# Performance work log

Hardware: AMD Instinct MI355X
Metric: run time of the kernel (lower is better)

## Reference

```python
import jax, jax.numpy as jnp
import numpy as np
from jax import lax

B, N, D, H, K = 8, 1024, 384, 6, 7
HD = D // H
EPS = 1e-5


def layer_norm(x, g, b):
    m = jnp.mean(x, axis=-1, keepdims=True)
    v = jnp.mean(jnp.square(x - m), axis=-1, keepdims=True)
    return (x - m) * lax.rsqrt(v + EPS) * g + b


def setup_inputs() -> dict:
    key = jax.random.key(0)
    ks = jax.random.split(key, 12)
    s = 0.02
    return {
        "x": jax.random.normal(ks[0], (B, N, D), jnp.float32),
        "qkv_w": jax.random.normal(ks[1], (3 * D, D), jnp.float32) * s,
        "qkv_b": jnp.zeros((3 * D,), jnp.float32),
        "proj_w": jax.random.normal(ks[2], (D, D), jnp.float32) * s,
        "proj_b": jnp.zeros((D,), jnp.float32),
        "t_before": jnp.eye(H, dtype=jnp.float32) + jax.random.normal(ks[3], (H, H), jnp.float32) * 0.01,
        "t_after": jnp.eye(H, dtype=jnp.float32) + jax.random.normal(ks[4], (H, H), jnp.float32) * 0.01,
        "dw_w": jax.random.normal(ks[5], (D, 1, K), jnp.float32) * s,
        "dw_b": jnp.zeros((D,), jnp.float32),
        "mlp_ln_g": jnp.ones((D,), jnp.float32),
        "mlp_ln_b": jnp.zeros((D,), jnp.float32),
        "norm1_g": jnp.ones((D,), jnp.float32),
        "norm1_b": jnp.zeros((D,), jnp.float32),
        "norm2_g": jnp.ones((D,), jnp.float32),
        "norm2_b": jnp.zeros((D,), jnp.float32),
        "fc1_w": jax.random.normal(ks[6], (4 * D, D), jnp.float32) * s,
        "fc1_b": jnp.zeros((4 * D,), jnp.float32),
        "fc2_w": jax.random.normal(ks[7], (D, 4 * D), jnp.float32) * s,
        "fc2_b": jnp.zeros((D,), jnp.float32),
    }


def reference(x, qkv_w, qkv_b, proj_w, proj_b, t_before, t_after, dw_w, dw_b,
              mlp_ln_g, mlp_ln_b, norm1_g, norm1_b, norm2_g, norm2_b,
              fc1_w, fc1_b, fc2_w, fc2_b):
    # ---- attention branch ----
    h = layer_norm(x, norm1_g, norm1_b)
    qkv = h @ qkv_w.T + qkv_b                                  # (B,N,3D)
    qkv = qkv.reshape(B, N, 3, H, HD).transpose(2, 0, 3, 1, 4)  # (3,B,H,N,hd)
    q, k, v = qkv[0], qkv[1], qkv[2]
    scale = HD ** -0.5
    scores = jnp.einsum('bhnd,bhmd->bhnm', q, k) * scale        # (B,H,N,N)
    scores = jnp.einsum('gh,bhnm->bgnm', t_before, scores)       # head-mix pre-softmax
    probs = jax.nn.softmax(scores, axis=-1)
    probs = jnp.einsum('gh,bhnm->bgnm', t_after, probs)          # head-mix post-softmax
    attn_out = jnp.einsum('bhnm,bhmd->bhnd', probs, v)           # (B,H,N,hd)
    attn_out = attn_out.transpose(0, 2, 1, 3).reshape(B, N, D)
    attn_out = attn_out @ proj_w.T + proj_b
    x = x + attn_out
    # ---- MLP branch ----
    h = layer_norm(x, norm2_g, norm2_b)
    # depthwise conv1d over tokens: (B,D,N), groups=D, same padding
    h_t = h.transpose(0, 2, 1)
    h_t = lax.conv_general_dilated(h_t, dw_w, window_strides=(1,),
                                   padding=[(K // 2, K // 2)],
                                   dimension_numbers=('NCH', 'OIH', 'NCH'),
                                   feature_group_count=D)
    h = h_t.transpose(0, 2, 1) + dw_b
    h = layer_norm(h, mlp_ln_g, mlp_ln_b)
    h = jax.nn.gelu(h @ fc1_w.T + fc1_b, approximate=False)
    h = h @ fc2_w.T + fc2_b
    return x + h
```

## Files before the change

kernel.cpp:

```cpp
#include <hip/hip_runtime.h>
#include <hip/hip_bf16.h>

#define BB 8
#define NN 1024
#define DD 384
#define HH 6
#define HD 64
#define BN 8192
#define D3 1152
#define D4 1536
#define SEC 3145728

typedef __attribute__((ext_vector_type(8))) short short8;
typedef __attribute__((ext_vector_type(4))) float f32x4;
typedef __attribute__((ext_vector_type(2))) float f32x2;
typedef long v2i64 __attribute__((ext_vector_type(2)));

typedef __attribute__((address_space(3))) unsigned char as3_byte;
typedef __attribute__((address_space(1))) const unsigned char as1_byte;

__device__ __forceinline__ void gload16(const void* g, void* l){
  __builtin_amdgcn_global_load_lds((as1_byte*)g, (as3_byte*)l, 16, 0, 0);
}

__device__ __forceinline__ float b2f(unsigned short u){
  union{unsigned int i; float f;} x; x.i=((unsigned int)u)<<16; return x.f;
}
__device__ __forceinline__ unsigned short f2b(float f){
  unsigned int u=__float_as_uint(f);
  return (unsigned short)((u + 0x7FFFu + ((u>>16)&1u))>>16);
}
__device__ __forceinline__ unsigned char f2f8(float f){
  return (unsigned char)(__builtin_amdgcn_cvt_pk_fp8_f32(f, f, 0, false) & 0xff);
}

__global__ void cvt_kernel(const float* __restrict__ w0, const float* __restrict__ w1,
                           const float* __restrict__ w2, const float* __restrict__ w3,
                           unsigned char* __restrict__ out8){
  int i = blockIdx.x*256 + threadIdx.x;
  if (i < 442368)        out8[i] = f2f8(w0[i]*8.0f);
  else if (i < 589824)   out8[i] = f2f8(w1[i - 442368]*8.0f);
  else if (i < 1179648)  out8[i] = f2f8(w2[i - 589824]*8.0f);
  else if (i < 1769472)  out8[i] = f2f8(w3[i - 1179648]*8.0f);
}

template<int OUT8>
__global__ __launch_bounds__(128)
void ln_kernel(const float* __restrict__ in, const float* __restrict__ gg, const float* __restrict__ bb,
               unsigned short* __restrict__ outb, unsigned char* __restrict__ out8){
  int row = blockIdx.x, t = threadIdx.x;
  const float* r = in + (size_t)row*DD;
  float v0=r[t], v1=r[t+128], v2=r[t+256];
  float s=v0+v1+v2, q=v0*v0+v1*v1+v2*v2;
  #pragma unroll
  for (int o=32;o>0;o>>=1){ s+=__shfl_down(s,o); q+=__shfl_down(q,o); }
  __shared__ float ls[2], lq[2];
  if ((t&63)==0){ ls[t>>6]=s; lq[t>>6]=q; }
  __syncthreads();
  float S=ls[0]+ls[1], Q=lq[0]+lq[1];
  float mean=S*(1.0f/DD);
  float rstd=rsqrtf(Q*(1.0f/DD)-mean*mean+1e-5f);
  float o0=(v0-mean)*rstd*gg[t]+bb[t];
  float o1=(v1-mean)*rstd*gg[t+128]+bb[t+128];
  float o2=(v2-mean)*rstd*gg[t+256]+bb[t+256];
  if (OUT8){
    unsigned char* o=out8+(size_t)row*DD;
    o[t]=f2f8(o0*4.0f); o[t+128]=f2f8(o1*4.0f); o[t+256]=f2f8(o2*4.0f);
  } else {
    unsigned short* o=outb+(size_t)row*DD;
    o[t]=f2b(o0); o[t+128]=f2b(o1); o[t+256]=f2b(o2);
  }
}

__global__ __launch_bounds__(128)
void conv_ln_kernel(const unsigned short* __restrict__ h2, const float* __restrict__ dww, const float* __restrict__ dwb,
                    const float* __restrict__ gg, const float* __restrict__ bb, unsigned char* __restrict__ out8){
  int row=blockIdx.x, t=threadIdx.x;
  int bi=row>>10, n=row&1023;
  const unsigned short* base = h2 + (size_t)(bi<<10)*DD;
  float a[3];
  #pragma unroll
  for (int j=0;j<3;j++){
    int d=t+j*128;
    float acc=dwb[d];
    #pragma unroll
    for (int k=0;k<7;k++){
      int nn=n+k-3;
      if (nn>=0 && nn<NN) acc += dww[d*7+k]*b2f(base[(size_t)nn*DD + d]);
    }
    a[j]=acc;
  }
  float s=a[0]+a[1]+a[2], q=a[0]*a[0]+a[1]*a[1]+a[2]*a[2];
  #pragma unroll
  for (int o=32;o>0;o>>=1){ s+=__shfl_down(s,o); q+=__shfl_down(q,o); }
  __shared__ float ls[2], lq[2];
  if ((t&63)==0){ ls[t>>6]=s; lq[t>>6]=q; }
  __syncthreads();
  float S=ls[0]+ls[1], Q=lq[0]+lq[1];
  float mean=S*(1.0f/DD);
  float rstd=rsqrtf(Q*(1.0f/DD)-mean*mean+1e-5f);
  unsigned char* o = out8 + (size_t)row*DD;
  #pragma unroll
  for (int j=0;j<3;j++){
    int d=t+j*128;
    o[d]=f2f8(((a[j]-mean)*rstd*gg[d]+bb[d])*4.0f);
  }
}

template<int MODE>
__global__ __launch_bounds__(256)
void gemm8_kernel(const unsigned char* __restrict__ A8, const unsigned char* __restrict__ W8,
                  const float* __restrict__ bias, const float* __restrict__ resid,
                  float* __restrict__ outf, unsigned char* __restrict__ out8,
                  unsigned char* __restrict__ qk8out, unsigned char* __restrict__ v8out,
                  int Kdim, int Ncols){
  __shared__ __align__(16) unsigned char As[2][64*64];
  __shared__ __align__(16) unsigned char Bs[2][64*64];
  int t=threadIdx.x, lane=t&63, w=t>>6;
  int bm = blockIdx.x*64;
  int bn = blockIdx.y*64;
  int wr = w>>1, wc = w&1;
  int c16=lane&15, r16=lane>>4;
  f32x4 acc[2][2] = {};
  int arow = t>>2, aslot = (t&3) ^ (arow&3);
  auto stage = [&](int buf, int k0){
    gload16(A8 + (size_t)(bm+arow)*Kdim + k0 + aslot*16, (char*)As + buf*4096 + t*16);
    gload16(W8 + (size_t)(bn+arow)*Kdim + k0 + aslot*16, (char*)Bs + buf*4096 + t*16);
  };
  int niter = Kdim>>6;
  stage(0, 0);
  __syncthreads();
  for (int it=0; it<niter; ++it){
    if (it+1<niter) stage((it+1)&1, (it+1)<<6);
    int off = (it&1)*4096;
    #pragma unroll
    for (int kk=0;kk<2;kk++){
      long afr[2], bfr[2];
      #pragma unroll
      for (int i=0;i<2;i++){
        int ra = wr*32 + i*16 + c16;
        int sa = (kk*2 + (r16>>1)) ^ (ra&3);
        afr[i] = *(const long*)((char*)As + off + ra*64 + (sa<<4) + ((r16&1)<<3));
        int rb = wc*32 + i*16 + c16;
        int sb = (kk*2 + (r16>>1)) ^ (rb&3);
        bfr[i] = *(const long*)((char*)Bs + off + rb*64 + (sb<<4) + ((r16&1)<<3));
      }
      #pragma unroll
      for (int i=0;i<2;i++)
        #pragma unroll
        for (int j=0;j<2;j++)
          acc[i][j] = __builtin_amdgcn_mfma_f32_16x16x32_fp8_fp8(afr[i], bfr[j], acc[i][j], 0,0,0);
    }
    __syncthreads();
  }
  #pragma unroll
  for (int i=0;i<2;i++)
    #pragma unroll
    for (int j=0;j<2;j++)
      #pragma unroll
      for (int r=0;r<4;r++){
        int row = bm + wr*32 + i*16 + r16*4 + r;
        int col = bn + wc*32 + j*16 + c16;
        float v = acc[i][j][r]*0.03125f + bias[col];
        if (MODE==0){
          int c = col/384; int rem = col - c*384; int hh = rem>>6, d = rem&63;
          int bi = row>>10, nn = row&1023;
          unsigned char pk = f2f8(v);
          if (c==2){
            v8out[(((size_t)(bi*6+hh))<<16) + ((size_t)d<<10) + nn] = pk;
          } else {
            size_t fa = ((size_t)c*SEC)
                      + ((((size_t)(bi*6+hh))<<6) + (nn>>4))*1024
                      + ((((d>>3)&3)*16 + (nn&15))<<4) + ((d>>5)*8) + (d&7);
            qk8out[fa] = pk;
          }
        } else if (MODE==1){
          size_t idx = (size_t)row*Ncols + col;
          outf[idx] = resid[idx] + v;
        } else {
          float ge = 0.5f*v*(1.0f+erff(v*0.70710678118654752f));
          out8[(size_t)row*Ncols + col] = f2f8(ge*4.0f);
        }
      }
}

__global__ __launch_bounds__(256, 4)
void smx_kernel(const unsigned char* __restrict__ qk8, const float* __restrict__ tbm,
                unsigned char* __restrict__ E, float* __restrict__ lpart){
  __shared__ float lred[4][6][16];
  int t=threadIdx.x, lane=t&63, w=t>>6;
  int blk=blockIdx.x;
  int b = blk&7, nt = (blk>>3)&63, mh = blk>>9;
  int n0 = nt*16, mbase = mh*512;
  int c16=lane&15, r16=lane>>4;
  const unsigned char* q8f = qk8;
  const unsigned char* k8f = qk8 + SEC;
  v2i64 qf[6];
  #pragma unroll
  for (int h=0;h<6;h++)
    qf[h] = *(const v2i64*)(q8f + (((((size_t)(b*6+h))<<6) + (n0>>4))<<10) + lane*16);
  float tbr[36];
  #pragma unroll
  for (int i=0;i<36;i++) tbr[i] = tbm[i];
  const float SC = 0.125f*1.44269504088896f;
  float lsum[6]={0.f,0.f,0.f,0.f,0.f,0.f};
  #pragma unroll
  for (int mt=0; mt<4; ++mt){
    int m0a = mbase + mt*128 + w*16;
    int m0b = m0a + 64;
    v2i64 kfa[6], kfb[6];
    #pragma unroll
    for (int h=0;h<6;h++)
      kfa[h] = *(const v2i64*)(k8f + (((((size_t)(b*6+h))<<6) + (m0a>>4))<<10) + lane*16);
    #pragma unroll
    for (int h=0;h<6;h++)
      kfb[h] = *(const v2i64*)(k8f + (((((size_t)(b*6+h))<<6) + (m0b>>4))<<10) + lane*16);
    {
      f32x4 aq[6] = {};
      #pragma unroll
      for (int h=0;h<6;h++){
        aq[h] = __builtin_amdgcn_mfma_f32_16x16x32_fp8_fp8(kfa[h][0], qf[h][0], aq[h], 0,0,0);
        aq[h] = __builtin_amdgcn_mfma_f32_16x16x32_fp8_fp8(kfa[h][1], qf[h][1], aq[h], 0,0,0);
      }
      #pragma unroll
      for (int g=0;g<6;g++){
        float e0,e1,e2,e3;
        {
          float sm;
          sm = tbr[g*6]*aq[0][0]+tbr[g*6+1]*aq[1][0]+tbr[g*6+2]*aq[2][0]
             + tbr[g*6+3]*aq[3][0]+tbr[g*6+4]*aq[4][0]+tbr[g*6+5]*aq[5][0];
          e0 = __builtin_amdgcn_exp2f(sm*SC);
          sm = tbr[g*6]*aq[0][1]+tbr[g*6+1]*aq[1][1]+tbr[g*6+2]*aq[2][1]
             + tbr[g*6+3]*aq[3][1]+tbr[g*6+4]*aq[4][1]+tbr[g*6+5]*aq[5][1];
          e1 = __builtin_amdgcn_exp2f(sm*SC);
          sm = tbr[g*6]*aq[0][2]+tbr[g*6+1]*aq[1][2]+tbr[g*6+2]*aq[2][2]
             + tbr[g*6+3]*aq[3][2]+tbr[g*6+4]*aq[4][2]+tbr[g*6+5]*aq[5][2];
          e2 = __builtin_amdgcn_exp2f(sm*SC);
          sm = tbr[g*6]*aq[0][3]+tbr[g*6+1]*aq[1][3]+tbr[g*6+2]*aq[2][3]
             + tbr[g*6+3]*aq[3][3]+tbr[g*6+4]*aq[4][3]+tbr[g*6+5]*aq[5][3];
          e3 = __builtin_amdgcn_exp2f(sm*SC);
        }
        lsum[g] += (e0+e1)+(e2+e3);
        int pkv = __builtin_amdgcn_cvt_pk_fp8_f32(e0, e1, 0, false);
        pkv = __builtin_amdgcn_cvt_pk_fp8_f32(e2, e3, pkv, true);
        *(unsigned int*)(E + (((size_t)(b*6+g))<<20) + ((size_t)(n0+c16)<<10) + m0a + r16*4)
          = (unsigned int)pkv;
      }
    }
    {
      f32x4 aq[6] = {};
      #pragma unroll
      for (int h=0;h<6;h++){
        aq[h] = __builtin_amdgcn_mfma_f32_16x16x32_fp8_fp8(kfb[h][0], qf[h][0], aq[h], 0,0,0);
        aq[h] = __builtin_amdgcn_mfma_f32_16x16x32_fp8_fp8(kfb[h][1], qf[h][1], aq[h], 0,0,0);
      }
      #pragma unroll
      for (int g=0;g<6;g++){
        float e0,e1,e2,e3;
        {
          float sm;
          sm = tbr[g*6]*aq[0][0]+tbr[g*6+1]*aq[1][0]+tbr[g*6+2]*aq[2][0]
             + tbr[g*6+3]*aq[3][0]+tbr[g*6+4]*aq[4][0]+tbr[g*6+5]*aq[5][0];
          e0 = __builtin_amdgcn_exp2f(sm*SC);
          sm = tbr[g*6]*aq[0][1]+tbr[g*6+1]*aq[1][1]+tbr[g*6+2]*aq[2][1]
             + tbr[g*6+3]*aq[3][1]+tbr[g*6+4]*aq[4][1]+tbr[g*6+5]*aq[5][1];
          e1 = __builtin_amdgcn_exp2f(sm*SC);
          sm = tbr[g*6]*aq[0][2]+tbr[g*6+1]*aq[1][2]+tbr[g*6+2]*aq[2][2]
             + tbr[g*6+3]*aq[3][2]+tbr[g*6+4]*aq[4][2]+tbr[g*6+5]*aq[5][2];
          e2 = __builtin_amdgcn_exp2f(sm*SC);
          sm = tbr[g*6]*aq[0][3]+tbr[g*6+1]*aq[1][3]+tbr[g*6+2]*aq[2][3]
             + tbr[g*6+3]*aq[3][3]+tbr[g*6+4]*aq[4][3]+tbr[g*6+5]*aq[5][3];
          e3 = __builtin_amdgcn_exp2f(sm*SC);
        }
        lsum[g] += (e0+e1)+(e2+e3);
        int pkv = __builtin_amdgcn_cvt_pk_fp8_f32(e0, e1, 0, false);
        pkv = __builtin_amdgcn_cvt_pk_fp8_f32(e2, e3, pkv, true);
        *(unsigned int*)(E + (((size_t)(b*6+g))<<20) + ((size_t)(n0+c16)<<10) + m0b + r16*4)
          = (unsigned int)pkv;
      }
    }
  }
  #pragma unroll
  for (int g=0;g<6;g++){
    lsum[g] += __shfl_xor(lsum[g],16);
    lsum[g] += __shfl_xor(lsum[g],32);
  }
  if (r16==0){
    #pragma unroll
    for (int g=0;g<6;g++) lred[w][g][c16] = lsum[g];
  }
  __syncthreads();
  if (w==0 && r16==0){
    #pragma unroll
    for (int g=0;g<6;g++){
      float l = lred[0][g][c16]+lred[1][g][c16]+lred[2][g][c16]+lred[3][g][c16];
      lpart[(((size_t)(mh*48 + b*6+g))<<10) + n0 + c16] = l;
    }
  }
}

__global__ __launch_bounds__(256, 2)
void pvmix_kernel(const unsigned char* __restrict__ E, const unsigned char* __restrict__ V8,
                  const float* __restrict__ lpart, const float* __restrict__ tam,
                  unsigned char* __restrict__ outp8){
  __shared__ __align__(16) unsigned char Es[6*16*64];
  __shared__ __align__(16) unsigned char Vs[6*64*64];
  __shared__ __align__(16) unsigned char pms[6*16*64];
  int t=threadIdx.x, lane=t&63, w=t>>6;
  int b = blockIdx.x&7, nt = blockIdx.x>>3;
  int n0 = nt*16;
  int c16 = lane&15, r16 = lane>>4;
  int mn = t&15, mg = (t>>4)&7, gh = t>>7;
  float cf[3][6];
  #pragma unroll
  for (int g=0;g<6;g++){
    float l0 = lpart[(((size_t)(b*6+g))<<10) + n0 + mn];
    float l1 = lpart[(((size_t)(48 + b*6+g))<<10) + n0 + mn];
    float iv = 256.0f/(l0 + l1);
    #pragma unroll
    for (int j=0;j<3;j++) cf[j][g] = tam[(gh*3+j)*6 + g]*iv;
  }
  auto stageE = [&](int m0){
    #pragma unroll
    for (int i=0;i<2;i++){
      int u = t + i*256;
      if (u<384){
        int r = u>>2, s = (u&3) ^ (r&3);
        int g = r>>4, n = r&15;
        gload16(E + (((size_t)(b*6+g))<<20) + ((size_t)(n0+n)<<10) + m0 + s*16,
                (char*)Es + u*16);
      }
    }
  };
  auto stageV = [&](int m0){
    #pragma unroll
    for (int i=0;i<6;i++){
      int u = t + i*256;
      int r = u>>2, s = (u&3) ^ (r&3);
      int g = r>>6, d = r&63;
      gload16(V8 + (((size_t)(b*6+g))<<16) + ((size_t)d<<10) + m0 + s*16,
              (char*)Vs + u*16);
    }
  };
  stageE(0); stageV(0);
  __syncthreads();
  f32x4 acc[6] = {};
  for (int mt=0; mt<16; ++mt){
    float e[6][8];
    #pragma unroll
    for (int g=0;g<6;g++){
      int row = g*16 + mn;
      int byteo = row*64 + ((mg*8) ^ ((row&3)<<4));
      unsigned int lo = *(const unsigned int*)(Es + byteo);
      unsigned int hi = *(const unsigned int*)(Es + byteo + 4);
      f32x2 p0 = __builtin_amdgcn_cvt_pk_f32_fp8(lo, false);
      f32x2 p1 = __builtin_amdgcn_cvt_pk_f32_fp8(lo, true);
      f32x2 p2 = __builtin_amdgcn_cvt_pk_f32_fp8(hi, false);
      f32x2 p3 = __builtin_amdgcn_cvt_pk_f32_fp8(hi, true);
      e[g][0]=p0.x; e[g][1]=p0.y; e[g][2]=p1.x; e[g][3]=p1.y;
      e[g][4]=p2.x; e[g][5]=p2.y; e[g][6]=p3.x; e[g][7]=p3.y;
    }
    #pragma unroll
    for (int j=0;j<3;j++){
      float pm[8];
      #pragma unroll
      for (int m=0;m<8;m++)
        pm[m] = cf[j][0]*e[0][m]+cf[j][1]*e[1][m]+cf[j][2]*e[2][m]
              + cf[j][3]*e[3][m]+cf[j][4]*e[4][m]+cf[j][5]*e[5][m];
      int d0 = __builtin_amdgcn_cvt_pk_fp8_f32(pm[0], pm[1], 0, false);
      d0 = __builtin_amdgcn_cvt_pk_fp8_f32(pm[2], pm[3], d0, true);
      int d1 = __builtin_amdgcn_cvt_pk_fp8_f32(pm[4], pm[5], 0, false);
      d1 = __builtin_amdgcn_cvt_pk_fp8_f32(pm[6], pm[7], d1, true);
      int prow = (gh*3+j)*16 + mn;
      int pbyte = prow*64 + ((mg*8) ^ ((mn&7)<<3));
      *(unsigned int*)(pms + pbyte)     = (unsigned int)d0;
      *(unsigned int*)(pms + pbyte + 4) = (unsigned int)d1;
    }
    __syncthreads();
    if (mt<15) stageE((mt+1)*64);
    #pragma unroll
    for (int g=0;g<6;g++){
      int arow = g*16 + c16;
      int vrow = g*64 + w*16 + c16;
      #pragma unroll
      for (int kk=0;kk<2;kk++){
        long af = *(const long*)(pms + arow*64 + ((kk*32 + r16*8) ^ ((c16&7)<<3)));
        long bf = *(const long*)(Vs + vrow*64
                   + ((((kk*2 + (r16>>1)) ^ (vrow&3))<<4) + ((r16&1)<<3)));
        acc[g] = __builtin_amdgcn_mfma_f32_16x16x32_fp8_fp8(af, bf, acc[g], 0,0,0);
      }
    }
    __syncthreads();
    if (mt<15) stageV((mt+1)*64);
  }
  #pragma unroll
  for (int g=0;g<6;g++)
    #pragma unroll
    for (int r=0;r<4;r++){
      int n = n0 + r16*4 + r;
      int d = g*64 + w*16 + c16;
      outp8[((size_t)(b*1024 + n))*DD + d] = f2f8(acc[g][r] * 0.015625f);
    }
}

extern "C" void kernel_launch(void* const* d_in, const int* in_sizes, int n_in,
                              void* d_out, int out_size, void* d_ws, size_t ws_size,
                              hipStream_t stream){
  const float* x      = (const float*)d_in[0];
  const float* qkv_w  = (const float*)d_in[1];
  const float* qkv_b  = (const float*)d_in[2];
  const float* proj_w = (const float*)d_in[3];
  const float* proj_b = (const float*)d_in[4];
  const float* t_before=(const float*)d_in[5];
  const float* t_after =(const float*)d_in[6];
  const float* dw_w   = (const float*)d_in[7];
  const float* dw_b   = (const float*)d_in[8];
  const float* mlp_g  = (const float*)d_in[9];
  const float* mlp_b  = (const float*)d_in[10];
  const float* n1_g   = (const float*)d_in[11];
  const float* n1_b   = (const float*)d_in[12];
  const float* n2_g   = (const float*)d_in[13];
  const float* n2_b   = (const float*)d_in[14];
  const float* fc1_w  = (const float*)d_in[15];
  const float* fc1_b  = (const float*)d_in[16];
  const float* fc2_w  = (const float*)d_in[17];
  const float* fc2_b  = (const float*)d_in[18];
  float* out = (float*)d_out;
  char* ws = (char*)d_ws;
  unsigned char*  qkvw8 = (unsigned char*)(ws + 0);
  unsigned char*  projw8= (unsigned char*)(ws + 442368);
  unsigned char*  fc1w8 = (unsigned char*)(ws + 589824);
  unsigned char*  fc2w8 = (unsigned char*)(ws + 1179648);
  unsigned char*  hb8   = (unsigned char*)(ws + 1769472);
  unsigned char*  qk8   = (unsigned char*)(ws + 4915200);
  unsigned char*  V8    = (unsigned char*)(ws + 11206656);
  float*          lpart = (float*)        (ws + 14352384);
  unsigned char*  Ebuf  = (unsigned char*)(ws + 14745600);
  unsigned char*  attnb8= (unsigned char*)(ws + 65077248);
  float*          x2    = (float*)        (ws + 68222976);
  unsigned short* h2 = (unsigned short*)qk8;
  unsigned char*  hcln8 = hb8;
  unsigned char*  fc1o8 = Ebuf;

  cvt_kernel<<<6912,256,0,stream>>>(qkv_w, proj_w, fc1_w, fc2_w, qkvw8);

  ln_kernel<1><<<BN,128,0,stream>>>(x, n1_g, n1_b, nullptr, hb8);
  { dim3 g(BN/64, D3/64); gemm8_kernel<0><<<g,256,0,stream>>>(hb8, qkvw8, qkv_b, nullptr, nullptr, nullptr, qk8, V8, DD, D3); }
  smx_kernel<<<1024,256,0,stream>>>(qk8, t_before, Ebuf, lpart);
  pvmix_kernel<<<512,256,0,stream>>>(Ebuf, V8, lpart, t_after, attnb8);
  { dim3 g(BN/64, DD/64); gemm8_kernel<1><<<g,256,0,stream>>>(attnb8, projw8, proj_b, x, x2, nullptr, nullptr, nullptr, DD, DD); }
  ln_kernel<0><<<BN,128,0,stream>>>(x2, n2_g, n2_b, h2, nullptr);
  conv_ln_kernel<<<BN,128,0,stream>>>(h2, dw_w, dw_b, mlp_g, mlp_b, hcln8);
  { dim3 g(BN/64, D4/64); gemm8_kernel<2><<<g,256,0,stream>>>(hcln8, fc1w8, fc1_b, nullptr, nullptr, fc1o8, nullptr, nullptr, DD, D4); }
  { dim3 g(BN/64, DD/64); gemm8_kernel<1><<<g,256,0,stream>>>(fc1o8, fc2w8, fc2_b, x2, out, nullptr, nullptr, nullptr, D4, DD); }
}
```

Measured before the change: 186.5 us.

## Fuse softmax and PV kernels into one two-pass attention kernel recomputing QK

Merges the separate score/exp kernel and the head-mix/PV kernel into a single kernel. A first pass computes QK scores and only the row sums of exp. A second pass recomputes the scores per 64-column tile, normalizes them, applies the post-softmax head mix and feeds the PV MFMA directly. This removes the large fp8 E buffer write and read (about 50MB) and the lpart round trip. In exchange QK MFMAs and exps are done twice, and the grid halves from 1024 to 512 blocks, which lowers parallelism in the first pass.

```diff
diff --git a/kernel.cpp b/kernel.cpp
--- a/kernel.cpp
+++ b/kernel.cpp
@@ -184,14 +184,16 @@
       }
 }
 
-__global__ __launch_bounds__(256, 4)
-void smx_kernel(const unsigned char* __restrict__ qk8, const float* __restrict__ tbm,
-                unsigned char* __restrict__ E, float* __restrict__ lpart){
+__global__ __launch_bounds__(256, 2)
+void fattn8_kernel(const unsigned char* __restrict__ qk8, const unsigned char* __restrict__ V8,
+                   const float* __restrict__ tbm, const float* __restrict__ tam,
+                   unsigned char* __restrict__ outp8){
+  __shared__ __align__(16) unsigned char Vs[6*64*64];
+  __shared__ __align__(16) unsigned char pms[6*16*64];
   __shared__ float lred[4][6][16];
   int t=threadIdx.x, lane=t&63, w=t>>6;
-  int blk=blockIdx.x;
-  int b = blk&7, nt = (blk>>3)&63, mh = blk>>9;
-  int n0 = nt*16, mbase = mh*512;
+  int b = blockIdx.x&7, nt = blockIdx.x>>3;
+  int n0 = nt*16;
   int c16=lane&15, r16=lane>>4;
   const unsigned char* q8f = qk8;
   const unsigned char* k8f = qk8 + SEC;
@@ -199,14 +201,14 @@
   #pragma unroll
   for (int h=0;h<6;h++)
     qf[h] = *(const v2i64*)(q8f + (((((size_t)(b*6+h))<<6) + (n0>>4))<<10) + lane*16);
-  float tbr[36];
-  #pragma unroll
-  for (int i=0;i<36;i++) tbr[i] = tbm[i];
+  float tbr[36], tar[36];
+  #pragma unroll
+  for (int i=0;i<36;i++){ tbr[i]=tbm[i]; tar[i]=tam[i]; }
   const float SC = 0.125f*1.44269504088896f;
   float lsum[6]={0.f,0.f,0.f,0.f,0.f,0.f};
   #pragma unroll
-  for (int mt=0; mt<4; ++mt){
-    int m0a = mbase + mt*128 + w*16;
+  for (int mt=0; mt<8; ++mt){
+    int m0a = mt*128 + w*16;
     int m0b = m0a + 64;
     v2i64 kfa[6], kfb[6];
     #pragma unroll
@@ -223,28 +225,15 @@
         aq[h] = __builtin_amdgcn_mfma_f32_16x16x32_fp8_fp8(kfa[h][1], qf[h][1], aq[h], 0,0,0);
       }
       #pragma unroll
-      for (int g=0;g<6;g++){
-        float e0,e1,e2,e3;
-        {
-          float sm;
-          sm = tbr[g*6]*aq[0][0]+tbr[g*6+1]*aq[1][0]+tbr[g*6+2]*aq[2][0]
-             + tbr[g*6+3]*aq[3][0]+tbr[g*6+4]*aq[4][0]+tbr[g*6+5]*aq[5][0];
-          e0 = __builtin_amdgcn_exp2f(sm*SC);
-          sm = tbr[g*6]*aq[0][1]+tbr[g*6+1]*aq[1][1]+tbr[g*6+2]*aq[2][1]
-             + tbr[g*6+3]*aq[3][1]+tbr[g*6+4]*aq[4][1]+tbr[g*6+5]*aq[5][1];
-          e1 = __builtin_amdgcn_exp2f(sm*SC);
-          sm = tbr[g*6]*aq[0][2]+tbr[g*6+1]*aq[1][2]+tbr[g*6+2]*aq[2][2]
-             + tbr[g*6+3]*aq[3][2]+tbr[g*6+4]*aq[4][2]+tbr[g*6+5]*aq[5][2];
-          e2 = __builtin_amdgcn_exp2f(sm*SC);
-          sm = tbr[g*6]*aq[0][3]+tbr[g*6+1]*aq[1][3]+tbr[g*6+2]*aq[2][3]
-             + tbr[g*6+3]*aq[3][3]+tbr[g*6+4]*aq[4][3]+tbr[g*6+5]*aq[5][3];
-          e3 = __builtin_amdgcn_exp2f(sm*SC);
+      for (int r=0;r<4;r++){
+        float s0=aq[0][r], s1=aq[1][r], s2=aq[2][r],
+              s3=aq[3][r], s4=aq[4][r], s5=aq[5][r];
+        #pragma unroll
+        for (int g=0;g<6;g++){
+          float sm = tbr[g*6]*s0 + tbr[g*6+1]*s1 + tbr[g*6+2]*s2
+                   + tbr[g*6+3]*s3 + tbr[g*6+4]*s4 + tbr[g*6+5]*s5;
+          lsum[g] += __builtin_amdgcn_exp2f(sm*SC);
         }
-        lsum[g] += (e0+e1)+(e2+e3);
-        int pkv = __builtin_amdgcn_cvt_pk_fp8_f32(e0, e1, 0, false);
-        pkv = __builtin_amdgcn_cvt_pk_fp8_f32(e2, e3, pkv, true);
-        *(unsigned int*)(E + (((size_t)(b*6+g))<<20) + ((size_t)(n0+c16)<<10) + m0a + r16*4)
-          = (unsigned int)pkv;
       }
     }
     {
@@ -255,28 +244,15 @@
         aq[h] = __builtin_amdgcn_mfma_f32_16x16x32_fp8_fp8(kfb[h][1], qf[h][1], aq[h], 0,0,0);
       }
       #pragma unroll
-      for (int g=0;g<6;g++){
-        float e0,e1,e2,e3;
-        {
-          float sm;
-          sm = tbr[g*6]*aq[0][0]+tbr[g*6+1]*aq[1][0]+tbr[g*6+2]*aq[2][0]
-             + tbr[g*6+3]*aq[3][0]+tbr[g*6+4]*aq[4][0]+tbr[g*6+5]*aq[5][0];
-          e0 = __builtin_amdgcn_exp2f(sm*SC);
-          sm = tbr[g*6]*aq[0][1]+tbr[g*6+1]*aq[1][1]+tbr[g*6+2]*aq[2][1]
-             + tbr[g*6+3]*aq[3][1]+tbr[g*6+4]*aq[4][1]+tbr[g*6+5]*aq[5][1];
-          e1 = __builtin_amdgcn_exp2f(sm*SC);
-          sm = tbr[g*6]*aq[0][2]+tbr[g*6+1]*aq[1][2]+tbr[g*6+2]*aq[2][2]
-             + tbr[g*6+3]*aq[3][2]+tbr[g*6+4]*aq[4][2]+tbr[g*6+5]*aq[5][2];
-          e2 = __builtin_amdgcn_exp2f(sm*SC);
-          sm = tbr[g*6]*aq[0][3]+tbr[g*6+1]*aq[1][3]+tbr[g*6+2]*aq[2][3]
-             + tbr[g*6+3]*aq[3][3]+tbr[g*6+4]*aq[4][3]+tbr[g*6+5]*aq[5][3];
-          e3 = __builtin_amdgcn_exp2f(sm*SC);
+      for (int r=0;r<4;r++){
+        float s0=aq[0][r], s1=aq[1][r], s2=aq[2][r],
+              s3=aq[3][r], s4=aq[4][r], s5=aq[5][r];
+        #pragma unroll
+        for (int g=0;g<6;g++){
+          float sm = tbr[g*6]*s0 + tbr[g*6+1]*s1 + tbr[g*6+2]*s2
+                   + tbr[g*6+3]*s3 + tbr[g*6+4]*s4 + tbr[g*6+5]*s5;
+          lsum[g] += __builtin_amdgcn_exp2f(sm*SC);
         }
-        lsum[g] += (e0+e1)+(e2+e3);
-        int pkv = __builtin_amdgcn_cvt_pk_fp8_f32(e0, e1, 0, false);
-        pkv = __builtin_amdgcn_cvt_pk_fp8_f32(e2, e3, pkv, true);
-        *(unsigned int*)(E + (((size_t)(b*6+g))<<20) + ((size_t)(n0+c16)<<10) + m0b + r16*4)
-          = (unsigned int)pkv;
       }
     }
   }
@@ -290,48 +266,10 @@
     for (int g=0;g<6;g++) lred[w][g][c16] = lsum[g];
   }
   __syncthreads();
-  if (w==0 && r16==0){
-    #pragma unroll
-    for (int g=0;g<6;g++){
-      float l = lred[0][g][c16]+lred[1][g][c16]+lred[2][g][c16]+lred[3][g][c16];
-      lpart[(((size_t)(mh*48 + b*6+g))<<10) + n0 + c16] = l;
-    }
-  }
-}
-
-__global__ __launch_bounds__(256, 2)
-void pvmix_kernel(const unsigned char* __restrict__ E, const unsigned char* __restrict__ V8,
-                  const float* __restrict__ lpart, const float* __restrict__ tam,
-                  unsigned char* __restrict__ outp8){
-  __shared__ __align__(16) unsigned char Es[6*16*64];
-  __shared__ __align__(16) unsigned char Vs[6*64*64];
-  __shared__ __align__(16) unsigned char pms[6*16*64];
-  int t=threadIdx.x, lane=t&63, w=t>>6;
-  int b = blockIdx.x&7, nt = blockIdx.x>>3;
-  int n0 = nt*16;
-  int c16 = lane&15, r16 = lane>>4;
-  int mn = t&15, mg = (t>>4)&7, gh = t>>7;
-  float cf[3][6];
-  #pragma unroll
-  for (int g=0;g<6;g++){
-    float l0 = lpart[(((size_t)(b*6+g))<<10) + n0 + mn];
-    float l1 = lpart[(((size_t)(48 + b*6+g))<<10) + n0 + mn];
-    float iv = 256.0f/(l0 + l1);
-    #pragma unroll
-    for (int j=0;j<3;j++) cf[j][g] = tam[(gh*3+j)*6 + g]*iv;
-  }
-  auto stageE = [&](int m0){
-    #pragma unroll
-    for (int i=0;i<2;i++){
-      int u = t + i*256;
-      if (u<384){
-        int r = u>>2, s = (u&3) ^ (r&3);
-        int g = r>>4, n = r&15;
-        gload16(E + (((size_t)(b*6+g))<<20) + ((size_t)(n0+n)<<10) + m0 + s*16,
-                (char*)Es + u*16);
-      }
-    }
-  };
+  float invl[6];
+  #pragma unroll
+  for (int g=0;g<6;g++)
+    invl[g] = 256.0f/(lred[0][g][c16]+lred[1][g][c16]+lred[2][g][c16]+lred[3][g][c16]);
   auto stageV = [&](int m0){
     #pragma unroll
     for (int i=0;i<6;i++){
@@ -342,42 +280,46 @@
               (char*)Vs + u*16);
     }
   };
-  stageE(0); stageV(0);
+  stageV(0);
   __syncthreads();
   f32x4 acc[6] = {};
+  int pmoff = (((w*2+(r16>>1))<<3) ^ ((c16&7)<<3)) + ((r16&1)<<2);
   for (int mt=0; mt<16; ++mt){
-    float e[6][8];
-    #pragma unroll
-    for (int g=0;g<6;g++){
-      int row = g*16 + mn;
-      int byteo = row*64 + ((mg*8) ^ ((row&3)<<4));
-      unsigned int lo = *(const unsigned int*)(Es + byteo);
-      unsigned int hi = *(const unsigned int*)(Es + byteo + 4);
-      f32x2 p0 = __builtin_amdgcn_cvt_pk_f32_fp8(lo, false);
-      f32x2 p1 = __builtin_amdgcn_cvt_pk_f32_fp8(lo, true);
-      f32x2 p2 = __builtin_amdgcn_cvt_pk_f32_fp8(hi, false);
-      f32x2 p3 = __builtin_amdgcn_cvt_pk_f32_fp8(hi, true);
-      e[g][0]=p0.x; e[g][1]=p0.y; e[g][2]=p1.x; e[g][3]=p1.y;
-      e[g][4]=p2.x; e[g][5]=p2.y; e[g][6]=p3.x; e[g][7]=p3.y;
-    }
-    #pragma unroll
-    for (int j=0;j<3;j++){
-      float pm[8];
-      #pragma unroll
-      for (int m=0;m<8;m++)
-        pm[m] = cf[j][0]*e[0][m]+cf[j][1]*e[1][m]+cf[j][2]*e[2][m]
-              + cf[j][3]*e[3][m]+cf[j][4]*e[4][m]+cf[j][5]*e[5][m];
-      int d0 = __builtin_amdgcn_cvt_pk_fp8_f32(pm[0], pm[1], 0, false);
-      d0 = __builtin_amdgcn_cvt_pk_fp8_f32(pm[2], pm[3], d0, true);
-      int d1 = __builtin_amdgcn_cvt_pk_fp8_f32(pm[4], pm[5], 0, false);
-      d1 = __builtin_amdgcn_cvt_pk_fp8_f32(pm[6], pm[7], d1, true);
-      int prow = (gh*3+j)*16 + mn;
-      int pbyte = prow*64 + ((mg*8) ^ ((mn&7)<<3));
-      *(unsigned int*)(pms + pbyte)     = (unsigned int)d0;
-      *(unsigned int*)(pms + pbyte + 4) = (unsigned int)d1;
+    int m0 = mt*64 + w*16;
+    v2i64 kf[6];
+    #pragma unroll
+    for (int h=0;h<6;h++)
+      kf[h] = *(const v2i64*)(k8f + (((((size_t)(b*6+h))<<6) + (m0>>4))<<10) + lane*16);
+    f32x4 aq[6] = {};
+    #pragma unroll
+    for (int h=0;h<6;h++){
+      aq[h] = __builtin_amdgcn_mfma_f32_16x16x32_fp8_fp8(kf[h][0], qf[h][0], aq[h], 0,0,0);
+      aq[h] = __builtin_amdgcn_mfma_f32_16x16x32_fp8_fp8(kf[h][1], qf[h][1], aq[h], 0,0,0);
+    }
+    float pm[6][4];
+    #pragma unroll
+    for (int r=0;r<4;r++){
+      float s0=aq[0][r], s1=aq[1][r], s2=aq[2][r],
+            s3=aq[3][r], s4=aq[4][r], s5=aq[5][r];
+      float eg[6];
+      #pragma unroll
+      for (int g=0;g<6;g++){
+        float sm = tbr[g*6]*s0 + tbr[g*6+1]*s1 + tbr[g*6+2]*s2
+                 + tbr[g*6+3]*s3 + tbr[g*6+4]*s4 + tbr[g*6+5]*s5;
+        eg[g] = __builtin_amdgcn_exp2f(sm*SC) * invl[g];
+      }
+      #pragma unroll
+      for (int g2=0;g2<6;g2++)
+        pm[g2][r] = tar[g2*6]*eg[0] + tar[g2*6+1]*eg[1] + tar[g2*6+2]*eg[2]
+                  + tar[g2*6+3]*eg[3] + tar[g2*6+4]*eg[4] + tar[g2*6+5]*eg[5];
+    }
+    #pragma unroll
+    for (int g2=0;g2<6;g2++){
+      int d0 = __builtin_amdgcn_cvt_pk_fp8_f32(pm[g2][0], pm[g2][1], 0, false);
+      d0 = __builtin_amdgcn_cvt_pk_fp8_f32(pm[g2][2], pm[g2][3], d0, true);
+      *(unsigned int*)(pms + (g2*16 + c16)*64 + pmoff) = (unsigned int)d0;
     }
     __syncthreads();
-    if (mt<15) stageE((mt+1)*64);
     #pragma unroll
     for (int g=0;g<6;g++){
       int arow = g*16 + c16;
@@ -434,20 +376,17 @@
   unsigned char*  hb8   = (unsigned char*)(ws + 1769472);
   unsigned char*  qk8   = (unsigned char*)(ws + 4915200);
   unsigned char*  V8    = (unsigned char*)(ws + 11206656);
-  float*          lpart = (float*)        (ws + 14352384);
-  unsigned char*  Ebuf  = (unsigned char*)(ws + 14745600);
+  unsigned char*  fc1o8 = (unsigned char*)(ws + 14745600);
   unsigned char*  attnb8= (unsigned char*)(ws + 65077248);
   float*          x2    = (float*)        (ws + 68222976);
   unsigned short* h2 = (unsigned short*)qk8;
   unsigned char*  hcln8 = hb8;
-  unsigned char*  fc1o8 = Ebuf;
 
   cvt_kernel<<<6912,256,0,stream>>>(qkv_w, proj_w, fc1_w, fc2_w, qkvw8);
 
   ln_kernel<1><<<BN,128,0,stream>>>(x, n1_g, n1_b, nullptr, hb8);
   { dim3 g(BN/64, D3/64); gemm8_kernel<0><<<g,256,0,stream>>>(hb8, qkvw8, qkv_b, nullptr, nullptr, nullptr, qk8, V8, DD, D3); }
-  smx_kernel<<<1024,256,0,stream>>>(qk8, t_before, Ebuf, lpart);
-  pvmix_kernel<<<512,256,0,stream>>>(Ebuf, V8, lpart, t_after, attnb8);
+  fattn8_kernel<<<512,256,0,stream>>>(qk8, V8, t_before, t_after, attnb8);
   { dim3 g(BN/64, DD/64); gemm8_kernel<1><<<g,256,0,stream>>>(attnb8, projw8, proj_b, x, x2, nullptr, nullptr, nullptr, DD, DD); }
   ln_kernel<0><<<BN,128,0,stream>>>(x2, n2_g, n2_b, h2, nullptr);
   conv_ln_kernel<<<BN,128,0,stream>>>(h2, dw_w, dw_b, mlp_g, mlp_b, hcln8);
```

After: 183.8 us. Within noise of the previous version (-1.4%).
